# Kernel tuning notes

Hardware: AMD Instinct MI355X
Metric: run time of the kernel (lower is better)

Reference implementation:

```python
import jax, jax.numpy as jnp
import numpy as np

VOCAB, D = 50257, 768
B, S = 8, 2048
THRESHOLD = 0.01
MASK_SCALE = 0.02
INIT_SPARSITY = 0.1


def setup_inputs() -> dict:
    key = jax.random.key(0)
    k_x, k_m, k_w = jax.random.split(key, 3)
    x = jax.random.randint(k_x, (B, S), 0, VOCAB, dtype=jnp.int32)
    # mask_real ~ U(-mask_scale, (mask_scale+threshold)/initial_sparsity - mask_scale)
    lo = -MASK_SCALE
    hi = (MASK_SCALE + THRESHOLD) / INIT_SPARSITY - MASK_SCALE
    mask_real = jax.random.uniform(k_m, (VOCAB, D), dtype=jnp.float32, minval=lo, maxval=hi)
    weight = jax.random.normal(k_w, (VOCAB, D), dtype=jnp.float32)
    return {"x": x, "mask_real": mask_real, "weight": weight}


def reference(x, mask_real, weight):
    # Binarizer: 1 where mask_real > threshold, else 0 (le -> 0, gt -> 1)
    mask = jnp.where(mask_real > THRESHOLD, jnp.float32(1.0), jnp.float32(0.0)).astype(mask_real.dtype)
    weight_thresholded = mask * weight  # [V, D]
    return weight_thresholded[x]        # gather -> [B, S, D]
```

## Files before the change

### kernel.cpp

```cpp
#include <hip/hip_runtime.h>


#define D_DIM 768
#define D4 (D_DIM / 4)
#define THR 0.01f

__global__ __launch_bounds__(D4) void masked_embedding_kernel(
    const int* __restrict__ x,
    const float4* __restrict__ mask,
    const float4* __restrict__ weight,
    float4* __restrict__ out)
{
    const int token = blockIdx.x;
    const int col   = threadIdx.x;

    const int row = x[token];

    const size_t src = (size_t)row * D4 + col;
    const float4 m = mask[src];
    const float4 w = weight[src];

    float4 o;
    o.x = (m.x > THR) ? w.x : 0.0f;
    o.y = (m.y > THR) ? w.y : 0.0f;
    o.z = (m.z > THR) ? w.z : 0.0f;
    o.w = (m.w > THR) ? w.w : 0.0f;

    out[(size_t)token * D4 + col] = o;
}

extern "C" void kernel_launch(void* const* d_in, const int* in_sizes, int n_in,
                              void* d_out, int out_size, void* d_ws, size_t ws_size,
                              hipStream_t stream)
{
    const int*    x      = (const int*)d_in[0];
    const float4* mask   = (const float4*)d_in[1];
    const float4* weight = (const float4*)d_in[2];
    float4*       out    = (float4*)d_out;

    const int n_tokens = in_sizes[0];

    masked_embedding_kernel<<<n_tokens, D4, 0, stream>>>(x, mask, weight, out);
}
```

Before: 282.9 us.

## Map one wavefront per token with grid-stride loop and nontemporal stores

Replaces the one-block-per-token launch with a fixed grid of 2048 blocks of 256 threads. Each 64-lane wavefront handles one token per iteration, looping grid-stride over tokens, and each lane loads three float4 chunks of the mask and weight rows. The row index is made wave-uniform with readfirstlane, and output writes use nontemporal stores so they do not pollute the cache. This aims to cut block launch overhead and raise memory-level parallelism per thread, at the cost of depending on the grid size being well tuned.

Measured after the change: 281.0 us. No clear change (-0.7%).

```diff
diff --git a/kernel.cpp b/kernel.cpp
--- a/kernel.cpp
+++ b/kernel.cpp
@@ -2,43 +2,61 @@
 
 
 #define D_DIM 768
-#define D4 (D_DIM / 4)
-#define THR 0.01f
+#define D4    (D_DIM / 4)
+#define THR   0.01f
 
-__global__ __launch_bounds__(D4) void masked_embedding_kernel(
-    const int* __restrict__ x,
-    const float4* __restrict__ mask,
-    const float4* __restrict__ weight,
-    float4* __restrict__ out)
-{
-    const int token = blockIdx.x;
-    const int col   = threadIdx.x;
+typedef float f4 __attribute__((ext_vector_type(4)));
 
-    const int row = x[token];
-
-    const size_t src = (size_t)row * D4 + col;
-    const float4 m = mask[src];
-    const float4 w = weight[src];
-
-    float4 o;
+__device__ __forceinline__ f4 sel(f4 m, f4 w) {
+    f4 o;
     o.x = (m.x > THR) ? w.x : 0.0f;
     o.y = (m.y > THR) ? w.y : 0.0f;
     o.z = (m.z > THR) ? w.z : 0.0f;
     o.w = (m.w > THR) ? w.w : 0.0f;
+    return o;
+}
 
-    out[(size_t)token * D4 + col] = o;
+__global__ __launch_bounds__(256) void masked_embedding_kernel(
+    const int* __restrict__ x,
+    const f4*  __restrict__ mask,
+    const f4*  __restrict__ weight,
+    f4*        __restrict__ out,
+    int n_tokens)
+{
+    const int lane   = threadIdx.x & 63;
+    const int wid    = (blockIdx.x * blockDim.x + threadIdx.x) >> 6;
+    const int nwaves = (gridDim.x * blockDim.x) >> 6;
+
+    for (int token = wid; token < n_tokens; token += nwaves) {
+        const int row = __builtin_amdgcn_readfirstlane(x[token]);
+
+        const size_t base = (size_t)row   * D4 + lane;
+        const size_t ob   = (size_t)token * D4 + lane;
+
+        const f4 m0 = mask[base];
+        const f4 m1 = mask[base + 64];
+        const f4 m2 = mask[base + 128];
+        const f4 w0 = weight[base];
+        const f4 w1 = weight[base + 64];
+        const f4 w2 = weight[base + 128];
+
+        __builtin_nontemporal_store(sel(m0, w0), &out[ob]);
+        __builtin_nontemporal_store(sel(m1, w1), &out[ob + 64]);
+        __builtin_nontemporal_store(sel(m2, w2), &out[ob + 128]);
+    }
 }
 
 extern "C" void kernel_launch(void* const* d_in, const int* in_sizes, int n_in,
                               void* d_out, int out_size, void* d_ws, size_t ws_size,
                               hipStream_t stream)
 {
-    const int*    x      = (const int*)d_in[0];
-    const float4* mask   = (const float4*)d_in[1];
-    const float4* weight = (const float4*)d_in[2];
-    float4*       out    = (float4*)d_out;
+    const int* x      = (const int*)d_in[0];
+    const f4*  mask   = (const f4*)d_in[1];
+    const f4*  weight = (const f4*)d_in[2];
+    f4*        out    = (f4*)d_out;
 
     const int n_tokens = in_sizes[0];
 
-    masked_embedding_kernel<<<n_tokens, D4, 0, stream>>>(x, mask, weight, out);
+    const int blocks = 2048;
+    masked_embedding_kernel<<<blocks, 256, 0, stream>>>(x, mask, weight, out, n_tokens);
 }
```
